# Optimization experiments

Measured on AMD Instinct MI355X. Metric: run time of the kernel, lower is better.

The kernel has to match this reference:

```python
import jax, jax.numpy as jnp
import numpy as np

V, D, NH, HD, FF, NL, NLOOPS = 1056, 320, 5, 64, 864, 6, 8
CAP, EPS, THETA = 0.8, 1e-6, 10000.0
B, S = 8, 2048


def rmsnorm(x, w):
    return w * (x * jax.lax.rsqrt(jnp.mean(x * x, axis=-1, keepdims=True) + EPS))


def rotate_half(x):
    x1, x2 = jnp.split(x, 2, axis=-1)
    return jnp.concatenate([-x2, x1], axis=-1)


def rope_tables(seq_len):
    freqs = 1.0 / (THETA ** (jnp.arange(0, HD, 2, dtype=jnp.float32) / HD))  # [HD/2]
    t = jnp.arange(seq_len, dtype=jnp.float32)
    f = jnp.outer(t, freqs)                      # [S, HD/2]
    f = jnp.concatenate([f, f], axis=-1)         # [S, HD]
    return jnp.cos(f), jnp.sin(f)


def setup_inputs() -> dict:
    key = jax.random.key(0)
    ks = jax.random.split(key, 12)
    std = 0.02
    inp = {
        "input_ids": jax.random.randint(ks[0], (B, S), 0, V),
        "iteration": 0,
        "embedding": jax.random.normal(ks[1], (V, D), jnp.float32),
        "iter_emb": jax.random.normal(ks[2], (NLOOPS, D), jnp.float32),
        "attn_norm_w": jnp.ones((NL, D), jnp.float32),
        "Wqkv": jax.random.normal(ks[3], (NL, 3 * D, D), jnp.float32) * std,
        "wo_w": jax.random.normal(ks[4], (NL, D, D), jnp.float32) * std,
        "router_w": jax.random.normal(ks[5], (NL, D), jnp.float32) * std,
        "mlp_norm_w": jnp.ones((NL, D), jnp.float32),
        "gate_w": jax.random.normal(ks[6], (NL, FF, D), jnp.float32) * std,
        "up_w": jax.random.normal(ks[7], (NL, FF, D), jnp.float32) * std,
        "down_w": jax.random.normal(ks[8], (NL, D, FF), jnp.float32) * std,
        "final_norm_w": jnp.ones((D,), jnp.float32),
    }
    return inp


def reference(input_ids, iteration, embedding, iter_emb, attn_norm_w, Wqkv, wo_w,
              router_w, mlp_norm_w, gate_w, up_w, down_w, final_norm_w):
    batch, seq = input_ids.shape
    k = max(1, int(seq * CAP))
    cos, sin = rope_tables(seq)                 # [S, HD]
    cos4 = cos[None, :, None, :]                # [1,S,1,HD]
    sin4 = sin[None, :, None, :]

    x = embedding[input_ids]                    # [B,S,D]
    if iteration < NLOOPS:
        x = x + iter_emb[iteration][None, None, :]

    causal = jnp.tril(jnp.ones((seq, seq), dtype=bool))
    bidx = jnp.arange(batch)[:, None]           # [B,1]

    for l in range(NL):
        # --- attention block ---
        h = rmsnorm(x, attn_norm_w[l])
        qkv = (h @ Wqkv[l].T).reshape(batch, seq, 3, NH, HD)
        q, kk, v = qkv[:, :, 0], qkv[:, :, 1], qkv[:, :, 2]   # [B,S,H,HD]
        q = q * cos4 + rotate_half(q) * sin4
        kk = kk * cos4 + rotate_half(kk) * sin4
        q, kk, v = (t.transpose(0, 2, 1, 3) for t in (q, kk, v))  # [B,H,S,HD]
        scores = jnp.einsum("bhqd,bhkd->bhqk", q, kk) / np.sqrt(HD)
        scores = jnp.where(causal, scores, -jnp.inf)
        attn = jax.nn.softmax(scores, axis=-1)
        out = jnp.einsum("bhqk,bhkd->bhqd", attn, v)
        out = out.transpose(0, 2, 1, 3).reshape(batch, seq, D)
        x = x + out @ wo_w[l].T

        # --- MoD router + SwiGLU MLP on selected tokens ---
        probs = jax.nn.sigmoid(x @ router_w[l])            # [B,S]
        topk_probs, topk_idx = jax.lax.top_k(probs, k)     # [B,K]
        sel = jnp.take_along_axis(x, topk_idx[:, :, None], axis=1)  # [B,K,D]
        hs = rmsnorm(sel, mlp_norm_w[l])
        gate = jax.nn.silu(hs @ gate_w[l].T) * (hs @ up_w[l].T)
        mlp = (gate @ down_w[l].T) * topk_probs[:, :, None]         # [B,K,D]
        x = x.at[bidx, topk_idx].add(mlp)                  # unique idx: add == scatter-set+residual

    return rmsnorm(x, final_norm_w)
```

## Files before the change

kernel.cpp:

```cpp
#include <hip/hip_runtime.h>
#include <hip/hip_bf16.h>
#include <math.h>

#define VSZ 1056
#define DD 320
#define NH 5
#define HD 64
#define FF 864
#define NL 6
#define NLOOPS 8
#define BB 8
#define SL 2048
#define KK 1638
#define EPSF 1e-6f

typedef _Float16 f16x8 __attribute__((ext_vector_type(8)));
typedef _Float16 f16x4 __attribute__((ext_vector_type(4)));
typedef float floatx16 __attribute__((ext_vector_type(16)));

__device__ inline void gll16(const void* g, void* l) {
    __builtin_amdgcn_global_load_lds((const __attribute__((address_space(1))) void*)g,
                                     (__attribute__((address_space(3))) void*)l, 16, 0, 0);
}

__global__ __launch_bounds__(256) void cast4_kernel(const float* __restrict__ s,
        _Float16* __restrict__ d, int n4) {
    int i = blockIdx.x * 256 + threadIdx.x;
    if (i >= n4) return;
    float4 v = ((const float4*)s)[i];
    f16x4 o = { (_Float16)v.x, (_Float16)v.y, (_Float16)v.z, (_Float16)v.w };
    *(f16x4*)(d + (size_t)i * 4) = o;
}

__global__ __launch_bounds__(256) void rope_init_kernel(float2* __restrict__ tab) {
    int i = blockIdx.x * 256 + threadIdx.x;
    int s = i >> 5, j = i & 31;
    float freq = exp2f(-(float)j * 0.4152410118609203f);
    float ang = (float)s * freq;
    tab[i] = make_float2(cosf(ang), sinf(ang));
}

__global__ __launch_bounds__(256) void embed_kernel(const int* __restrict__ ids,
        const int* __restrict__ iter, const float* __restrict__ emb,
        const float* __restrict__ iter_emb, float* __restrict__ x) {
    int i = blockIdx.x * 256 + threadIdx.x;
    int d = i % DD, bs = i / DD;
    float v = emb[(size_t)ids[bs] * DD + d];
    int it = iter[0];
    if (it < NLOOPS) v += iter_emb[it * DD + d];
    x[i] = v;
}

template<typename OT>
__global__ __launch_bounds__(256) void rmsnorm_kernel(const float* __restrict__ x,
        const float* __restrict__ w, OT* __restrict__ out, int nrows) {
    int row = blockIdx.x * 4 + (threadIdx.x >> 6);
    int lane = threadIdx.x & 63;
    if (row >= nrows) return;
    const float* xr = x + (size_t)row * DD;
    float v[5]; float ss = 0.f;
#pragma unroll
    for (int i = 0; i < 5; ++i) { v[i] = xr[lane + i * 64]; ss += v[i] * v[i]; }
#pragma unroll
    for (int o = 32; o > 0; o >>= 1) ss += __shfl_xor(ss, o);
    float r = rsqrtf(ss * (1.f / DD) + EPSF);
    OT* orow = out + (size_t)row * DD;
#pragma unroll
    for (int i = 0; i < 5; ++i) orow[lane + i * 64] = (OT)(w[lane + i * 64] * v[i] * r);
}

__global__ __launch_bounds__(256) void gather_rmsnorm_kernel(const float* __restrict__ x,
        const int* __restrict__ tkidx, const float* __restrict__ w,
        _Float16* __restrict__ out, int nrows) {
    int row = blockIdx.x * 4 + (threadIdx.x >> 6);
    int lane = threadIdx.x & 63;
    if (row >= nrows) return;
    int b = row / KK;
    int t = tkidx[row];
    const float* xr = x + ((size_t)b * SL + t) * DD;
    float v[5]; float ss = 0.f;
#pragma unroll
    for (int i = 0; i < 5; ++i) { v[i] = xr[lane + i * 64]; ss += v[i] * v[i]; }
#pragma unroll
    for (int o = 32; o > 0; o >>= 1) ss += __shfl_xor(ss, o);
    float r = rsqrtf(ss * (1.f / DD) + EPSF);
    _Float16* orow = out + (size_t)row * DD;
#pragma unroll
    for (int i = 0; i < 5; ++i) orow[lane + i * 64] = (_Float16)(w[lane + i * 64] * v[i] * r);
}

__global__ __launch_bounds__(256) void router_kernel(const float* __restrict__ x,
        const float* __restrict__ rw, float* __restrict__ probs, int nrows) {
    int row = blockIdx.x * 4 + (threadIdx.x >> 6);
    int lane = threadIdx.x & 63;
    if (row >= nrows) return;
    const float* xr = x + (size_t)row * DD;
    float ss = 0.f;
#pragma unroll
    for (int i = 0; i < 5; ++i) ss += xr[lane + i * 64] * rw[lane + i * 64];
#pragma unroll
    for (int o = 32; o > 0; o >>= 1) ss += __shfl_xor(ss, o);
    if (lane == 0) probs[row] = 1.f / (1.f + __expf(-ss));
}

__global__ __launch_bounds__(1024) void topk_kernel(const float* __restrict__ probs,
        int* __restrict__ tkidx, float* __restrict__ tkprob) {
    __shared__ int hist[256];
    __shared__ int scn[256];
    __shared__ int outc;
    __shared__ int s_digit, s_rem;
    int b = blockIdx.x, tid = threadIdx.x;
    unsigned long long k0, k1;
    {
        unsigned int f0 = __float_as_uint(probs[b * SL + tid]);
        unsigned int f1 = __float_as_uint(probs[b * SL + tid + 1024]);
        k0 = ((unsigned long long)f0 << 32) | (unsigned int)(2047 - tid);
        k1 = ((unsigned long long)f1 << 32) | (unsigned int)(2047 - (tid + 1024));
    }
    if (tid == 0) outc = 0;
    unsigned long long prefix = 0, pmask = 0;
    int target = KK;
    for (int shift = 56; shift >= 0; shift -= 8) {
        if (tid < 256) hist[tid] = 0;
        __syncthreads();
        bool a0 = (k0 & pmask) == prefix;
        bool a1 = (k1 & pmask) == prefix;
        int d0 = (int)((k0 >> shift) & 255);
        int d1 = (int)((k1 >> shift) & 255);
        if (a0) atomicAdd(&hist[d0], 1);
        if (a1) atomicAdd(&hist[d1], 1);
        __syncthreads();
        if (tid < 256) scn[tid] = hist[tid];
        __syncthreads();
#pragma unroll
        for (int st = 1; st < 256; st <<= 1) {
            int v = 0;
            if (tid < 256 && tid + st < 256) v = scn[tid + st];
            __syncthreads();
            if (tid < 256) scn[tid] += v;
            __syncthreads();
        }
        if (tid < 256 && hist[tid] > 0) {
            int S = scn[tid];
            int Sgt = S - hist[tid];
            if (Sgt < target && target <= S) { s_digit = tid; s_rem = target - Sgt; }
        }
        __syncthreads();
        int dsel = s_digit, rem = s_rem;
        bool full = (rem == hist[dsel]);
        if (a0 && (d0 > dsel || (full && d0 == dsel))) {
            int s = atomicAdd(&outc, 1);
            tkidx[b * KK + s] = 2047 - (int)(k0 & 0xffffffffu);
            tkprob[b * KK + s] = __uint_as_float((unsigned int)(k0 >> 32));
        }
        if (a1 && (d1 > dsel || (full && d1 == dsel))) {
            int s = atomicAdd(&outc, 1);
            tkidx[b * KK + s] = 2047 - (int)(k1 & 0xffffffffu);
            tkprob[b * KK + s] = __uint_as_float((unsigned int)(k1 >> 32));
        }
        if (full) break;
        target = rem;
        prefix |= ((unsigned long long)dsel) << shift;
        pmask  |= ((unsigned long long)255) << shift;
        __syncthreads();
    }
}

__global__ __launch_bounds__(256) void prep_kernel(const _Float16* __restrict__ qkv,
        const float2* __restrict__ ropet,
        _Float16* __restrict__ Qh, _Float16* __restrict__ Kt, _Float16* __restrict__ Vt) {
    __shared__ _Float16 vt[64][72];
    int tid = threadIdx.x;
    int t = blockIdx.x, h = blockIdx.y, b = blockIdx.z;
    int bh = b * NH + h;
    int c = tid >> 5;
    int slb = tid & 31;
    const float QS = 0.125f * 1.44269504088896341f;
#pragma unroll
    for (int half = 0; half < 2; ++half) {
        int sl = half * 32 + slb;
        int s = t * 64 + sl;
        size_t rbase = ((size_t)(b * SL + s) * 3) * (NH * 64) + h * 64;
        f16x8 qv = *(const f16x8*)(qkv + rbase + c * 8);
        f16x8 qp = *(const f16x8*)(qkv + rbase + (c ^ 4) * 8);
        f16x8 kv = *(const f16x8*)(qkv + rbase + NH * 64 + c * 8);
        f16x8 kp = *(const f16x8*)(qkv + rbase + NH * 64 + (c ^ 4) * 8);
        f16x8 vv = *(const f16x8*)(qkv + rbase + 2 * NH * 64 + c * 8);
        const float2* rp = ropet + (size_t)s * 32 + (c & 3) * 8;
        f16x8 qo, ko;
#pragma unroll
        for (int j = 0; j < 8; ++j) {
            int d = c * 8 + j;
            float2 cs = rp[j];
            float cc = cs.x, sn = cs.y;
            float a = (float)qv[j], p = (float)qp[j];
            float ka = (float)kv[j], kb2 = (float)kp[j];
            float qr = (d < 32) ? a * cc - p * sn : a * cc + p * sn;
            float kr = (d < 32) ? ka * cc - kb2 * sn : ka * cc + kb2 * sn;
            qo[j] = (_Float16)(qr * QS);
            ko[j] = (_Float16)kr;
        }
        *(f16x8*)(Qh + ((size_t)bh * SL + s) * 64 + c * 8) = qo;
        *(f16x8*)(Kt + (((size_t)bh * 32 + t) * 8 + c) * 512 + sl * 8) = ko;
        *(f16x8*)(&vt[sl][c * 8]) = vv;
    }
    __syncthreads();
#pragma unroll
    for (int gg = 0; gg < 2; ++gg) {
        int oo = tid * 16 + gg * 8;
        int kc = oo >> 9;
        int d = (oo >> 3) & 63;
        f16x8 vo;
#pragma unroll
        for (int j = 0; j < 8; ++j) {
            int key = (kc >> 1) * 16 + (j & 3) + 8 * (j >> 2) + 4 * (kc & 1);
            vo[j] = vt[key][d];
        }
        *(f16x8*)(Vt + (((size_t)bh * 32 + t) * 8 + kc) * 512 + d * 8) = vo;
    }
}

__global__ __launch_bounds__(256, 2) void attn_mfma(const _Float16* __restrict__ Qh,
        const _Float16* __restrict__ Kt, const _Float16* __restrict__ Vt,
        _Float16* __restrict__ attn_out) {
    __shared__ float red[4][32][32];
    __shared__ float msh[4][32];
    __shared__ float lsh[4][32];
    int tid = threadIdx.x;
    int w = tid >> 6;
    int lane = tid & 63;
    int l31 = lane & 31, h5 = lane >> 5;
    int g = blockIdx.x;
    int j = g >> 3;
    int bh = (g & 7) + 8 * (j >> 5);
    int pr = j & 31;
    int b = bh / NH, h = bh % NH;

    const _Float16* Kb = Kt + (size_t)bh * 32 * 4096;
    const _Float16* Vb = Vt + (size_t)bh * 32 * 4096;

    for (int hf = 0; hf < 2; ++hf) {
        int qt = hf ? pr : 63 - pr;
        int nt = (qt >> 1) + 1;
        int qw = qt * 32;
        int myq = qw + l31;

        f16x8 qf[4];
        const _Float16* qrow = Qh + ((size_t)bh * SL + myq) * 64;
#pragma unroll
        for (int kd = 0; kd < 4; ++kd) qf[kd] = *(const f16x8*)(qrow + kd * 16 + h5 * 8);

        floatx16 O0, O1;
#pragma unroll
        for (int r = 0; r < 16; ++r) { O0[r] = 0.f; O1[r] = 0.f; }
        float m = -INFINITY, l = 0.f;

        for (int t = w; t < nt; t += 4) {
            const _Float16* kb = Kb + (size_t)t * 4096;
            const _Float16* vb = Vb + (size_t)t * 4096;
            f16x8 a0[4], a1[4], v0[4], v1[4];
#pragma unroll
            for (int kd = 0; kd < 4; ++kd) {
                int off = (kd * 2 + h5) * 512 + l31 * 8;
                a0[kd] = *(const f16x8*)(kb + off);
                a1[kd] = *(const f16x8*)(kb + off + 256);
            }
#pragma unroll
            for (int kc = 0; kc < 4; ++kc) {
                int off = (kc * 2 + h5) * 512 + l31 * 8;
                v0[kc] = *(const f16x8*)(vb + off);
                v1[kc] = *(const f16x8*)(vb + off + 256);
            }
            floatx16 S0, S1;
#pragma unroll
            for (int r = 0; r < 16; ++r) { S0[r] = 0.f; S1[r] = 0.f; }
#pragma unroll
            for (int kd = 0; kd < 4; ++kd) {
                S0 = __builtin_amdgcn_mfma_f32_32x32x16_f16(a0[kd], qf[kd], S0, 0, 0, 0);
                S1 = __builtin_amdgcn_mfma_f32_32x32x16_f16(a1[kd], qf[kd], S1, 0, 0, 0);
            }
            int t0 = t * 64;
            if (t0 + 63 > qw) {
#pragma unroll
                for (int r = 0; r < 16; ++r) {
                    int key = t0 + (r & 3) + 8 * (r >> 2) + 4 * h5;
                    if (key > myq) S0[r] = -INFINITY;
                    if (key + 32 > myq) S1[r] = -INFINITY;
                }
            }
            float tmax = S0[0];
#pragma unroll
            for (int r = 1; r < 16; ++r) tmax = fmaxf(tmax, S0[r]);
#pragma unroll
            for (int r = 0; r < 16; ++r) tmax = fmaxf(tmax, S1[r]);
            tmax = fmaxf(tmax, __shfl_xor(tmax, 32));
            if (__any(tmax > m + 8.f)) {
                float mnew = fmaxf(m, tmax);
                float alpha = exp2f(m - mnew);
                l *= alpha; O0 *= alpha; O1 *= alpha; m = mnew;
            }
            float P0[16], P1[16]; float psum = 0.f;
#pragma unroll
            for (int r = 0; r < 16; ++r) { P0[r] = exp2f(S0[r] - m); psum += P0[r]; }
#pragma unroll
            for (int r = 0; r < 16; ++r) { P1[r] = exp2f(S1[r] - m); psum += P1[r]; }
            psum += __shfl_xor(psum, 32);
            l += psum;
#pragma unroll
            for (int sub = 0; sub < 2; ++sub) {
                const float* P = sub ? P1 : P0;
#pragma unroll
                for (int kc = 0; kc < 2; ++kc) {
                    auto q01 = __builtin_amdgcn_cvt_pkrtz(P[kc * 8 + 0], P[kc * 8 + 1]);
                    auto q23 = __builtin_amdgcn_cvt_pkrtz(P[kc * 8 + 2], P[kc * 8 + 3]);
                    auto q45 = __builtin_amdgcn_cvt_pkrtz(P[kc * 8 + 4], P[kc * 8 + 5]);
                    auto q67 = __builtin_amdgcn_cvt_pkrtz(P[kc * 8 + 6], P[kc * 8 + 7]);
                    f16x8 pf;
                    pf[0] = (_Float16)q01[0]; pf[1] = (_Float16)q01[1];
                    pf[2] = (_Float16)q23[0]; pf[3] = (_Float16)q23[1];
                    pf[4] = (_Float16)q45[0]; pf[5] = (_Float16)q45[1];
                    pf[6] = (_Float16)q67[0]; pf[7] = (_Float16)q67[1];
                    int ksg = sub * 2 + kc;
                    O0 = __builtin_amdgcn_mfma_f32_32x32x16_f16(v0[ksg], pf, O0, 0, 0, 0);
                    O1 = __builtin_amdgcn_mfma_f32_32x32x16_f16(v1[ksg], pf, O1, 0, 0, 0);
                }
            }
        }
        if (h5 == 0) msh[w][l31] = m;
        __syncthreads();
        float M = fmaxf(fmaxf(msh[0][l31], msh[1][l31]), fmaxf(msh[2][l31], msh[3][l31]));
        float wgt = exp2f(m - M);
        if (h5 == 0) lsh[w][l31] = l * wgt;
#pragma unroll
        for (int r = 0; r < 16; ++r) {
            int d = (r & 3) + 8 * (r >> 2) + 4 * h5;
            red[w][d][l31] = O0[r] * wgt;
        }
        __syncthreads();
        float lsum = lsh[0][l31] + lsh[1][l31] + lsh[2][l31] + lsh[3][l31];
        float linv = 1.f / lsum;
        if (w < 2) {
            f16x8 ov;
#pragma unroll
            for (int k = 0; k < 8; ++k) {
                int d = w * 16 + h5 * 8 + k;
                ov[k] = (_Float16)((red[0][d][l31] + red[1][d][l31] +
                                    red[2][d][l31] + red[3][d][l31]) * linv);
            }
            *(f16x8*)(attn_out + ((size_t)(b * SL + myq)) * DD + h * 64 + w * 16 + h5 * 8) = ov;
        }
        __syncthreads();
#pragma unroll
        for (int r = 0; r < 16; ++r) {
            int d = (r & 3) + 8 * (r >> 2) + 4 * h5;
            red[w][d][l31] = O1[r] * wgt;
        }
        __syncthreads();
        if (w >= 2) {
            f16x8 ov;
#pragma unroll
            for (int k = 0; k < 8; ++k) {
                int d = (w - 2) * 16 + h5 * 8 + k;
                ov[k] = (_Float16)((red[0][d][l31] + red[1][d][l31] +
                                    red[2][d][l31] + red[3][d][l31]) * linv);
            }
            *(f16x8*)(attn_out + ((size_t)(b * SL + myq)) * DD + h * 64 + 32 + (w - 2) * 16 + h5 * 8) = ov;
        }
        __syncthreads();
    }
}

template<int MODE>
__global__ __launch_bounds__(256) void gemm_mfma(const _Float16* __restrict__ A,
        const _Float16* __restrict__ W, _Float16* __restrict__ Ch, float* __restrict__ X,
        int M, int N, int K, int nn_tiles, const int* __restrict__ sidx, const float* __restrict__ sprob) {
    __shared__ __attribute__((aligned(16))) _Float16 As[2][2048];
    __shared__ __attribute__((aligned(16))) _Float16 Ws[2][2048];
    int tid = threadIdx.x;
    int lane = tid & 63;
    int wave = tid >> 6;
    int l31 = lane & 31, h5 = lane >> 5;
    int nwg = gridDim.x;
    int q = nwg >> 3, r = nwg & 7;
    int xcd = blockIdx.x & 7, idx = blockIdx.x >> 3;
    int wgid = (xcd < r ? xcd * (q + 1) : r * (q + 1) + (xcd - r) * q) + idx;
    int mt = wgid / nn_tiles;
    int nt = wgid - mt * nn_tiles;
    int m0 = mt * 64, n0 = nt * 64;
    int wm = (wave & 1) * 32, wn = (wave >> 1) * 32;

    int srow = tid & 63;
    int skc = tid >> 6;
    int arow = m0 + srow; if (arow >= M) arow = M - 1;
    int wrow = n0 + srow; if (wrow >= N) wrow = N - 1;
    const _Float16* Ag = A + (size_t)arow * K + skc * 8;
    const _Float16* Wg = W + (size_t)wrow * K + skc * 8;
    _Float16* AsD = As[0] + (size_t)(tid & ~63) * 8;
    _Float16* WsD = Ws[0] + (size_t)(tid & ~63) * 8;

    floatx16 acc;
#pragma unroll
    for (int i = 0; i < 16; ++i) acc[i] = 0.f;

    gll16(Ag, AsD);
    gll16(Wg, WsD);
    __syncthreads();

    int nk = K >> 5;
    for (int t = 0; t < nk; ++t) {
        int buf = t & 1;
        if (t + 1 < nk) {
            int k0 = (t + 1) * 32;
            int bo = (buf ^ 1) * 2048;
            gll16(Ag + k0, AsD + bo);
            gll16(Wg + k0, WsD + bo);
        }
        const _Float16* Asb = As[buf];
        const _Float16* Wsb = Ws[buf];
#pragma unroll
        for (int ks = 0; ks < 2; ++ks) {
            int kc = ks * 2 + h5;
            f16x8 a = *(const f16x8*)(Asb + kc * 512 + (wm + l31) * 8);
            f16x8 b = *(const f16x8*)(Wsb + kc * 512 + (wn + l31) * 8);
            acc = __builtin_amdgcn_mfma_f32_32x32x16_f16(a, b, acc, 0, 0, 0);
        }
        __syncthreads();
    }

    int nn = n0 + wn + l31;
#pragma unroll
    for (int r2 = 0; r2 < 16; ++r2) {
        int mm = m0 + wm + (r2 & 3) + 8 * (r2 >> 2) + 4 * h5;
        if (mm >= M || nn >= N) continue;
        float v = acc[r2];
        if (MODE == 0) {
            Ch[(size_t)mm * N + nn] = (_Float16)v;
        } else if (MODE == 1) {
            X[(size_t)mm * N + nn] += v;
        } else {
            int b = mm / KK;
            X[((size_t)(b * SL + sidx[mm])) * N + nn] += v * sprob[mm];
        }
    }
}

__global__ __launch_bounds__(256) void gemm_gateup(const _Float16* __restrict__ A,
        const _Float16* __restrict__ Wg, const _Float16* __restrict__ Wu,
        _Float16* __restrict__ Ch, int M, int N, int K, int nn_tiles) {
    __shared__ __attribute__((aligned(16))) _Float16 As[2][2048];
    __shared__ __attribute__((aligned(16))) _Float16 Wgs[2][2048];
    __shared__ __attribute__((aligned(16))) _Float16 Wus[2][2048];
    int tid = threadIdx.x;
    int lane = tid & 63;
    int wave = tid >> 6;
    int l31 = lane & 31, h5 = lane >> 5;
    int nwg = gridDim.x;
    int q = nwg >> 3, r = nwg & 7;
    int xcd = blockIdx.x & 7, idx = blockIdx.x >> 3;
    int wgid = (xcd < r ? xcd * (q + 1) : r * (q + 1) + (xcd - r) * q) + idx;
    int mt = wgid / nn_tiles;
    int nt = wgid - mt * nn_tiles;
    int m0 = mt * 64, n0 = nt * 64;
    int wm = (wave & 1) * 32, wn = (wave >> 1) * 32;

    int srow = tid & 63;
    int skc = tid >> 6;
    int arow = m0 + srow; if (arow >= M) arow = M - 1;
    int wrow = n0 + srow; if (wrow >= N) wrow = N - 1;
    const _Float16* Ag  = A  + (size_t)arow * K + skc * 8;
    const _Float16* Wgg = Wg + (size_t)wrow * K + skc * 8;
    const _Float16* Wug = Wu + (size_t)wrow * K + skc * 8;
    _Float16* AsD  = As[0]  + (size_t)(tid & ~63) * 8;
    _Float16* WgsD = Wgs[0] + (size_t)(tid & ~63) * 8;
    _Float16* WusD = Wus[0] + (size_t)(tid & ~63) * 8;

    floatx16 ag, au;
#pragma unroll
    for (int i = 0; i < 16; ++i) { ag[i] = 0.f; au[i] = 0.f; }

    gll16(Ag, AsD);
    gll16(Wgg, WgsD);
    gll16(Wug, WusD);
    __syncthreads();

    int nk = K >> 5;
    for (int t = 0; t < nk; ++t) {
        int buf = t & 1;
        if (t + 1 < nk) {
            int k0 = (t + 1) * 32;
            int bo = (buf ^ 1) * 2048;
            gll16(Ag + k0, AsD + bo);
            gll16(Wgg + k0, WgsD + bo);
            gll16(Wug + k0, WusD + bo);
        }
        const _Float16* Asb = As[buf];
        const _Float16* Wgb = Wgs[buf];
        const _Float16* Wub = Wus[buf];
#pragma unroll
        for (int ks = 0; ks < 2; ++ks) {
            int kc = ks * 2 + h5;
            f16x8 a  = *(const f16x8*)(Asb + kc * 512 + (wm + l31) * 8);
            f16x8 g0 = *(const f16x8*)(Wgb + kc * 512 + (wn + l31) * 8);
            f16x8 u0 = *(const f16x8*)(Wub + kc * 512 + (wn + l31) * 8);
            ag = __builtin_amdgcn_mfma_f32_32x32x16_f16(a, g0, ag, 0, 0, 0);
            au = __builtin_amdgcn_mfma_f32_32x32x16_f16(a, u0, au, 0, 0, 0);
        }
        __syncthreads();
    }

    int nn = n0 + wn + l31;
#pragma unroll
    for (int r2 = 0; r2 < 16; ++r2) {
        int mm = m0 + wm + (r2 & 3) + 8 * (r2 >> 2) + 4 * h5;
        if (mm >= M || nn >= N) continue;
        float gv = ag[r2], uv = au[r2];
        Ch[(size_t)mm * N + nn] = (_Float16)((gv / (1.f + __expf(-gv))) * uv);
    }
}

extern "C" void kernel_launch(void* const* d_in, const int* in_sizes, int n_in,
                              void* d_out, int out_size, void* d_ws, size_t ws_size,
                              hipStream_t stream) {
    const int*   ids          = (const int*)d_in[0];
    const int*   iter         = (const int*)d_in[1];
    const float* emb          = (const float*)d_in[2];
    const float* iter_emb     = (const float*)d_in[3];
    const float* attn_norm_w  = (const float*)d_in[4];
    const float* Wqkv         = (const float*)d_in[5];
    const float* wo_w         = (const float*)d_in[6];
    const float* router_w     = (const float*)d_in[7];
    const float* mlp_norm_w   = (const float*)d_in[8];
    const float* gate_w       = (const float*)d_in[9];
    const float* up_w         = (const float*)d_in[10];
    const float* down_w       = (const float*)d_in[11];
    const float* final_norm_w = (const float*)d_in[12];
    float* out = (float*)d_out;

    const size_t XN   = (size_t)BB * SL * DD;
    const size_t QKVN = (size_t)BB * SL * 3 * DD;
    const size_t HN   = (size_t)BB * NH * SL * 64;
    char* ws = (char*)d_ws;
    size_t off = 0;
    float*    x        = (float*)(ws + off);    off += XN * 4;
    _Float16* h        = (_Float16*)(ws + off); off += XN * 2;
    _Float16* attn_out = (_Float16*)(ws + off); off += XN * 2;
    float*    probs    = (float*)(ws + off);    off += (size_t)BB * SL * 4;
    int*      tkidx    = (int*)(ws + off);      off += (size_t)BB * KK * 4;
    float*    tkprob   = (float*)(ws + off);    off += (size_t)BB * KK * 4;
    off = (off + 255) & ~(size_t)255;
    _Float16* qkvh     = (_Float16*)(ws + off); off += QKVN * 2;
    _Float16* Qh       = (_Float16*)(ws + off); off += HN * 2;
    _Float16* Kh       = (_Float16*)(ws + off); off += HN * 2;
    _Float16* Vh       = (_Float16*)(ws + off); off += HN * 2;
    float2*   ropet    = (float2*)(ws + off);   off += (size_t)SL * 32 * 8;
    _Float16* WqkvH    = (_Float16*)(ws + off);
    _Float16* woH   = WqkvH + (size_t)NL * 3 * DD * DD;
    _Float16* gateH = woH   + (size_t)NL * DD * DD;
    _Float16* upH   = gateH + (size_t)NL * FF * DD;
    _Float16* downH = upH   + (size_t)NL * FF * DD;
    _Float16* g1 = qkvh;

    rope_init_kernel<<<SL * 32 / 256, 256, 0, stream>>>(ropet);
    cast4_kernel<<<(NL * 3 * DD * DD / 4 + 255) / 256, 256, 0, stream>>>(Wqkv, WqkvH, NL * 3 * DD * DD / 4);
    cast4_kernel<<<(NL * DD * DD / 4 + 255) / 256, 256, 0, stream>>>(wo_w, woH, NL * DD * DD / 4);
    cast4_kernel<<<(NL * FF * DD / 4 + 255) / 256, 256, 0, stream>>>(gate_w, gateH, NL * FF * DD / 4);
    cast4_kernel<<<(NL * FF * DD / 4 + 255) / 256, 256, 0, stream>>>(up_w, upH, NL * FF * DD / 4);
    cast4_kernel<<<(NL * DD * FF / 4 + 255) / 256, 256, 0, stream>>>(down_w, downH, NL * DD * FF / 4);

    embed_kernel<<<20480, 256, 0, stream>>>(ids, iter, emb, iter_emb, x);

    const int M1 = BB * SL;
    const int M2 = BB * KK;
    const int MT1 = (M1 + 63) / 64;
    const int MT2 = (M2 + 63) / 64;
    for (int l = 0; l < NL; ++l) {
        rmsnorm_kernel<_Float16><<<4096, 256, 0, stream>>>(x, attn_norm_w + l * DD, h, M1);
        gemm_mfma<0><<<MT1 * 15, 256, 0, stream>>>(h, WqkvH + (size_t)l * 3 * DD * DD,
                                                   qkvh, nullptr, M1, 3 * DD, DD, 15, nullptr, nullptr);
        prep_kernel<<<dim3(SL / 64, NH, BB), 256, 0, stream>>>(qkvh, ropet, Qh, Kh, Vh);
        attn_mfma<<<BB * NH * (SL / 64), 256, 0, stream>>>(Qh, Kh, Vh, attn_out);
        gemm_mfma<1><<<MT1 * 5, 256, 0, stream>>>(attn_out, woH + (size_t)l * DD * DD,
                                                  nullptr, x, M1, DD, DD, 5, nullptr, nullptr);
        router_kernel<<<4096, 256, 0, stream>>>(x, router_w + l * DD, probs, M1);
        topk_kernel<<<BB, 1024, 0, stream>>>(probs, tkidx, tkprob);
        gather_rmsnorm_kernel<<<3276, 256, 0, stream>>>(x, tkidx, mlp_norm_w + l * DD, h, M2);
        gemm_gateup<<<MT2 * 14, 256, 0, stream>>>(h, gateH + (size_t)l * FF * DD,
                                                  upH + (size_t)l * FF * DD, g1, M2, FF, DD, 14);
        gemm_mfma<2><<<MT2 * 5, 256, 0, stream>>>(g1, downH + (size_t)l * DD * FF,
                                                  nullptr, x, M2, DD, FF, 5, tkidx, tkprob);
    }
    rmsnorm_kernel<float><<<4096, 256, 0, stream>>>(x, final_norm_w, out, M1);
}
```

Baseline: 1.604 ms.

## Split attention blocks per query tile, prefetch next K tile, raise MFMA priority

Each attention workgroup now handles a single 32-query tile instead of a balanced pair, so the grid doubles and tiles are ordered longest-first. The next K tile is loaded into registers while the current tile's softmax and PV MFMAs run, which is meant to hide global load latency. s_setprio brackets the MFMA sections so their waves get issue priority. The cost is higher register pressure from the prefetch buffers, and the causal workload is no longer pair-balanced per block.

New measurement: 1.587 ms. No clear change (-1.1%).

```diff
diff --git a/kernel.cpp b/kernel.cpp
--- a/kernel.cpp
+++ b/kernel.cpp
@@ -232,141 +232,155 @@
     int l31 = lane & 31, h5 = lane >> 5;
     int g = blockIdx.x;
     int j = g >> 3;
-    int bh = (g & 7) + 8 * (j >> 5);
-    int pr = j & 31;
+    int bh = (g & 7) + 8 * (j >> 6);
+    int qt = 63 - (j & 63);
     int b = bh / NH, h = bh % NH;
+    int nt = (qt >> 1) + 1;
+    int qw = qt * 32;
+    int myq = qw + l31;
+
+    f16x8 qf[4];
+    const _Float16* qrow = Qh + ((size_t)bh * SL + myq) * 64;
+#pragma unroll
+    for (int kd = 0; kd < 4; ++kd) qf[kd] = *(const f16x8*)(qrow + kd * 16 + h5 * 8);
 
     const _Float16* Kb = Kt + (size_t)bh * 32 * 4096;
     const _Float16* Vb = Vt + (size_t)bh * 32 * 4096;
 
-    for (int hf = 0; hf < 2; ++hf) {
-        int qt = hf ? pr : 63 - pr;
-        int nt = (qt >> 1) + 1;
-        int qw = qt * 32;
-        int myq = qw + l31;
-
-        f16x8 qf[4];
-        const _Float16* qrow = Qh + ((size_t)bh * SL + myq) * 64;
-#pragma unroll
-        for (int kd = 0; kd < 4; ++kd) qf[kd] = *(const f16x8*)(qrow + kd * 16 + h5 * 8);
-
-        floatx16 O0, O1;
-#pragma unroll
-        for (int r = 0; r < 16; ++r) { O0[r] = 0.f; O1[r] = 0.f; }
-        float m = -INFINITY, l = 0.f;
-
-        for (int t = w; t < nt; t += 4) {
-            const _Float16* kb = Kb + (size_t)t * 4096;
-            const _Float16* vb = Vb + (size_t)t * 4096;
-            f16x8 a0[4], a1[4], v0[4], v1[4];
-#pragma unroll
-            for (int kd = 0; kd < 4; ++kd) {
-                int off = (kd * 2 + h5) * 512 + l31 * 8;
-                a0[kd] = *(const f16x8*)(kb + off);
-                a1[kd] = *(const f16x8*)(kb + off + 256);
+    floatx16 O0, O1;
+#pragma unroll
+    for (int r = 0; r < 16; ++r) { O0[r] = 0.f; O1[r] = 0.f; }
+    float m = -INFINITY, l = 0.f;
+
+    f16x8 a0[4], a1[4];
+    {
+        const _Float16* kb0 = Kb + (size_t)w * 4096;
+#pragma unroll
+        for (int kd = 0; kd < 4; ++kd) {
+            int off = (kd * 2 + h5) * 512 + l31 * 8;
+            a0[kd] = *(const f16x8*)(kb0 + off);
+            a1[kd] = *(const f16x8*)(kb0 + off + 256);
+        }
+    }
+
+    for (int t = w; t < nt; t += 4) {
+        const _Float16* vb = Vb + (size_t)t * 4096;
+        f16x8 v0[4], v1[4];
+#pragma unroll
+        for (int kc = 0; kc < 4; ++kc) {
+            int off = (kc * 2 + h5) * 512 + l31 * 8;
+            v0[kc] = *(const f16x8*)(vb + off);
+            v1[kc] = *(const f16x8*)(vb + off + 256);
+        }
+        floatx16 S0, S1;
+#pragma unroll
+        for (int r = 0; r < 16; ++r) { S0[r] = 0.f; S1[r] = 0.f; }
+        __builtin_amdgcn_s_setprio(1);
+#pragma unroll
+        for (int kd = 0; kd < 4; ++kd) {
+            S0 = __builtin_amdgcn_mfma_f32_32x32x16_f16(a0[kd], qf[kd], S0, 0, 0, 0);
+            S1 = __builtin_amdgcn_mfma_f32_32x32x16_f16(a1[kd], qf[kd], S1, 0, 0, 0);
+        }
+        __builtin_amdgcn_s_setprio(0);
+        int tn = (t + 4 < nt) ? t + 4 : t;
+        const _Float16* kbn = Kb + (size_t)tn * 4096;
+        f16x8 na0[4], na1[4];
+#pragma unroll
+        for (int kd = 0; kd < 4; ++kd) {
+            int off = (kd * 2 + h5) * 512 + l31 * 8;
+            na0[kd] = *(const f16x8*)(kbn + off);
+            na1[kd] = *(const f16x8*)(kbn + off + 256);
+        }
+        int t0 = t * 64;
+        if (t0 + 63 > qw) {
+#pragma unroll
+            for (int r = 0; r < 16; ++r) {
+                int key = t0 + (r & 3) + 8 * (r >> 2) + 4 * h5;
+                if (key > myq) S0[r] = -INFINITY;
+                if (key + 32 > myq) S1[r] = -INFINITY;
             }
-#pragma unroll
-            for (int kc = 0; kc < 4; ++kc) {
-                int off = (kc * 2 + h5) * 512 + l31 * 8;
-                v0[kc] = *(const f16x8*)(vb + off);
-                v1[kc] = *(const f16x8*)(vb + off + 256);
+        }
+        float tmax = S0[0];
+#pragma unroll
+        for (int r = 1; r < 16; ++r) tmax = fmaxf(tmax, S0[r]);
+#pragma unroll
+        for (int r = 0; r < 16; ++r) tmax = fmaxf(tmax, S1[r]);
+        tmax = fmaxf(tmax, __shfl_xor(tmax, 32));
+        if (__any(tmax > m + 8.f)) {
+            float mnew = fmaxf(m, tmax);
+            float alpha = exp2f(m - mnew);
+            l *= alpha; O0 *= alpha; O1 *= alpha; m = mnew;
+        }
+        float P0[16], P1[16]; float psum = 0.f;
+#pragma unroll
+        for (int r = 0; r < 16; ++r) { P0[r] = exp2f(S0[r] - m); psum += P0[r]; }
+#pragma unroll
+        for (int r = 0; r < 16; ++r) { P1[r] = exp2f(S1[r] - m); psum += P1[r]; }
+        psum += __shfl_xor(psum, 32);
+        l += psum;
+        __builtin_amdgcn_s_setprio(1);
+#pragma unroll
+        for (int sub = 0; sub < 2; ++sub) {
+            const float* P = sub ? P1 : P0;
+#pragma unroll
+            for (int kc = 0; kc < 2; ++kc) {
+                auto q01 = __builtin_amdgcn_cvt_pkrtz(P[kc * 8 + 0], P[kc * 8 + 1]);
+                auto q23 = __builtin_amdgcn_cvt_pkrtz(P[kc * 8 + 2], P[kc * 8 + 3]);
+                auto q45 = __builtin_amdgcn_cvt_pkrtz(P[kc * 8 + 4], P[kc * 8 + 5]);
+                auto q67 = __builtin_amdgcn_cvt_pkrtz(P[kc * 8 + 6], P[kc * 8 + 7]);
+                f16x8 pf;
+                pf[0] = (_Float16)q01[0]; pf[1] = (_Float16)q01[1];
+                pf[2] = (_Float16)q23[0]; pf[3] = (_Float16)q23[1];
+                pf[4] = (_Float16)q45[0]; pf[5] = (_Float16)q45[1];
+                pf[6] = (_Float16)q67[0]; pf[7] = (_Float16)q67[1];
+                int ksg = sub * 2 + kc;
+                O0 = __builtin_amdgcn_mfma_f32_32x32x16_f16(v0[ksg], pf, O0, 0, 0, 0);
+                O1 = __builtin_amdgcn_mfma_f32_32x32x16_f16(v1[ksg], pf, O1, 0, 0, 0);
             }
-            floatx16 S0, S1;
-#pragma unroll
-            for (int r = 0; r < 16; ++r) { S0[r] = 0.f; S1[r] = 0.f; }
-#pragma unroll
-            for (int kd = 0; kd < 4; ++kd) {
-                S0 = __builtin_amdgcn_mfma_f32_32x32x16_f16(a0[kd], qf[kd], S0, 0, 0, 0);
-                S1 = __builtin_amdgcn_mfma_f32_32x32x16_f16(a1[kd], qf[kd], S1, 0, 0, 0);
-            }
-            int t0 = t * 64;
-            if (t0 + 63 > qw) {
-#pragma unroll
-                for (int r = 0; r < 16; ++r) {
-                    int key = t0 + (r & 3) + 8 * (r >> 2) + 4 * h5;
-                    if (key > myq) S0[r] = -INFINITY;
-                    if (key + 32 > myq) S1[r] = -INFINITY;
-                }
-            }
-            float tmax = S0[0];
-#pragma unroll
-            for (int r = 1; r < 16; ++r) tmax = fmaxf(tmax, S0[r]);
-#pragma unroll
-            for (int r = 0; r < 16; ++r) tmax = fmaxf(tmax, S1[r]);
-            tmax = fmaxf(tmax, __shfl_xor(tmax, 32));
-            if (__any(tmax > m + 8.f)) {
-                float mnew = fmaxf(m, tmax);
-                float alpha = exp2f(m - mnew);
-                l *= alpha; O0 *= alpha; O1 *= alpha; m = mnew;
-            }
-            float P0[16], P1[16]; float psum = 0.f;
-#pragma unroll
-            for (int r = 0; r < 16; ++r) { P0[r] = exp2f(S0[r] - m); psum += P0[r]; }
-#pragma unroll
-            for (int r = 0; r < 16; ++r) { P1[r] = exp2f(S1[r] - m); psum += P1[r]; }
-            psum += __shfl_xor(psum, 32);
-            l += psum;
-#pragma unroll
-            for (int sub = 0; sub < 2; ++sub) {
-                const float* P = sub ? P1 : P0;
-#pragma unroll
-                for (int kc = 0; kc < 2; ++kc) {
-                    auto q01 = __builtin_amdgcn_cvt_pkrtz(P[kc * 8 + 0], P[kc * 8 + 1]);
-                    auto q23 = __builtin_amdgcn_cvt_pkrtz(P[kc * 8 + 2], P[kc * 8 + 3]);
-                    auto q45 = __builtin_amdgcn_cvt_pkrtz(P[kc * 8 + 4], P[kc * 8 + 5]);
-                    auto q67 = __builtin_amdgcn_cvt_pkrtz(P[kc * 8 + 6], P[kc * 8 + 7]);
-                    f16x8 pf;
-                    pf[0] = (_Float16)q01[0]; pf[1] = (_Float16)q01[1];
-                    pf[2] = (_Float16)q23[0]; pf[3] = (_Float16)q23[1];
-                    pf[4] = (_Float16)q45[0]; pf[5] = (_Float16)q45[1];
-                    pf[6] = (_Float16)q67[0]; pf[7] = (_Float16)q67[1];
-                    int ksg = sub * 2 + kc;
-                    O0 = __builtin_amdgcn_mfma_f32_32x32x16_f16(v0[ksg], pf, O0, 0, 0, 0);
-                    O1 = __builtin_amdgcn_mfma_f32_32x32x16_f16(v1[ksg], pf, O1, 0, 0, 0);
-                }
-            }
-        }
-        if (h5 == 0) msh[w][l31] = m;
-        __syncthreads();
-        float M = fmaxf(fmaxf(msh[0][l31], msh[1][l31]), fmaxf(msh[2][l31], msh[3][l31]));
-        float wgt = exp2f(m - M);
-        if (h5 == 0) lsh[w][l31] = l * wgt;
-#pragma unroll
-        for (int r = 0; r < 16; ++r) {
-            int d = (r & 3) + 8 * (r >> 2) + 4 * h5;
-            red[w][d][l31] = O0[r] * wgt;
-        }
-        __syncthreads();
-        float lsum = lsh[0][l31] + lsh[1][l31] + lsh[2][l31] + lsh[3][l31];
-        float linv = 1.f / lsum;
-        if (w < 2) {
-            f16x8 ov;
-#pragma unroll
-            for (int k = 0; k < 8; ++k) {
-                int d = w * 16 + h5 * 8 + k;
-                ov[k] = (_Float16)((red[0][d][l31] + red[1][d][l31] +
-                                    red[2][d][l31] + red[3][d][l31]) * linv);
-            }
-            *(f16x8*)(attn_out + ((size_t)(b * SL + myq)) * DD + h * 64 + w * 16 + h5 * 8) = ov;
-        }
-        __syncthreads();
-#pragma unroll
-        for (int r = 0; r < 16; ++r) {
-            int d = (r & 3) + 8 * (r >> 2) + 4 * h5;
-            red[w][d][l31] = O1[r] * wgt;
-        }
-        __syncthreads();
-        if (w >= 2) {
-            f16x8 ov;
-#pragma unroll
-            for (int k = 0; k < 8; ++k) {
-                int d = (w - 2) * 16 + h5 * 8 + k;
-                ov[k] = (_Float16)((red[0][d][l31] + red[1][d][l31] +
-                                    red[2][d][l31] + red[3][d][l31]) * linv);
-            }
-            *(f16x8*)(attn_out + ((size_t)(b * SL + myq)) * DD + h * 64 + 32 + (w - 2) * 16 + h5 * 8) = ov;
-        }
-        __syncthreads();
+        }
+        __builtin_amdgcn_s_setprio(0);
+#pragma unroll
+        for (int kd = 0; kd < 4; ++kd) { a0[kd] = na0[kd]; a1[kd] = na1[kd]; }
+    }
+    if (h5 == 0) msh[w][l31] = m;
+    __syncthreads();
+    float M = fmaxf(fmaxf(msh[0][l31], msh[1][l31]), fmaxf(msh[2][l31], msh[3][l31]));
+    float wgt = exp2f(m - M);
+    if (h5 == 0) lsh[w][l31] = l * wgt;
+#pragma unroll
+    for (int r = 0; r < 16; ++r) {
+        int d = (r & 3) + 8 * (r >> 2) + 4 * h5;
+        red[w][d][l31] = O0[r] * wgt;
+    }
+    __syncthreads();
+    float lsum = lsh[0][l31] + lsh[1][l31] + lsh[2][l31] + lsh[3][l31];
+    float linv = 1.f / lsum;
+    if (w < 2) {
+        f16x8 ov;
+#pragma unroll
+        for (int k = 0; k < 8; ++k) {
+            int d = w * 16 + h5 * 8 + k;
+            ov[k] = (_Float16)((red[0][d][l31] + red[1][d][l31] +
+                                red[2][d][l31] + red[3][d][l31]) * linv);
+        }
+        *(f16x8*)(attn_out + ((size_t)(b * SL + myq)) * DD + h * 64 + w * 16 + h5 * 8) = ov;
+    }
+    __syncthreads();
+#pragma unroll
+    for (int r = 0; r < 16; ++r) {
+        int d = (r & 3) + 8 * (r >> 2) + 4 * h5;
+        red[w][d][l31] = O1[r] * wgt;
+    }
+    __syncthreads();
+    if (w >= 2) {
+        f16x8 ov;
+#pragma unroll
+        for (int k = 0; k < 8; ++k) {
+            int d = (w - 2) * 16 + h5 * 8 + k;
+            ov[k] = (_Float16)((red[0][d][l31] + red[1][d][l31] +
+                                red[2][d][l31] + red[3][d][l31]) * linv);
+        }
+        *(f16x8*)(attn_out + ((size_t)(b * SL + myq)) * DD + h * 64 + 32 + (w - 2) * 16 + h5 * 8) = ov;
     }
 }
 
@@ -578,7 +592,7 @@
         gemm_mfma<0><<<MT1 * 15, 256, 0, stream>>>(h, WqkvH + (size_t)l * 3 * DD * DD,
                                                    qkvh, nullptr, M1, 3 * DD, DD, 15, nullptr, nullptr);
         prep_kernel<<<dim3(SL / 64, NH, BB), 256, 0, stream>>>(qkvh, ropet, Qh, Kh, Vh);
-        attn_mfma<<<BB * NH * (SL / 64), 256, 0, stream>>>(Qh, Kh, Vh, attn_out);
+        attn_mfma<<<BB * NH * (SL / 32), 256, 0, stream>>>(Qh, Kh, Vh, attn_out);
         gemm_mfma<1><<<MT1 * 5, 256, 0, stream>>>(attn_out, woH + (size_t)l * DD * DD,
                                                   nullptr, x, M1, DD, DD, 5, nullptr, nullptr);
         router_kernel<<<4096, 256, 0, stream>>>(x, router_w + l * DD, probs, M1);
```
